# Performance work log

Measured on AMD Instinct MI355X. Metric: run time of the kernel, lower is better.

Reference implementation:

```python
import jax, jax.numpy as jnp
import numpy as np


def setup_inputs() -> dict:
    key = jax.random.key(0)
    k1, k2, k3, k4, k5 = jax.random.split(key, 5)
    D, K, W, C = 2048, 4096, 4096, 1000
    deep_feats = jax.random.normal(k1, (1, D), dtype=jnp.float32)
    cls_score = jax.random.normal(k2, (K, C), dtype=jnp.float32)
    target = jax.random.randint(k3, (1,), 0, C, dtype=jnp.int64)
    n = jax.random.normal(k4, (K, D), dtype=jnp.float32)
    w = jax.random.uniform(k5, (W, K), dtype=jnp.float32)
    return {"deep_feats": deep_feats, "cls_score": cls_score, "target": target, "n": n, "w": w}


def reference(deep_feats, cls_score, target, n, w):
    # d[idx] = ||deep_feats[0] - n[idx]||_2, shape [K]
    diff = deep_feats[0][None, :] - n            # [K, D]
    d = jnp.sqrt(jnp.sum(diff * diff, axis=-1))  # [K]
    # rho[idy] = softmax_idx(-w[idy] * d), shape [W, K]
    rho = jax.nn.softmax(-w * d[None, :], axis=-1)
    # f_loss = sum_{idy,idx} w[idy,idx] * d[idx]
    f_loss = jnp.sum(w * d[None, :])
    # per-neighbor cross entropy: ce[idx] = -log_softmax(cls_score[idx])[target]
    logp = jax.nn.log_softmax(cls_score, axis=-1)  # [K, C]
    ce = -logp[:, target[0]]                        # [K]
    # g_loss = sum_{idy,idx} rho[idy,idx] * ce[idx]
    g_loss = jnp.sum(rho @ ce)
    return g_loss + f_loss
```

## Files before the change

### kernel.cpp

```cpp
#include <hip/hip_runtime.h>
#include <math.h>

constexpr int KN = 4096;
constexpr int DN = 2048;
constexpr int CN = 1000;
constexpr int WN = 4096;

__device__ __forceinline__ float waveSum(float v) {
#pragma unroll
    for (int o = 32; o > 0; o >>= 1) v += __shfl_xor(v, o, 64);
    return v;
}
__device__ __forceinline__ float waveMax(float v) {
#pragma unroll
    for (int o = 32; o > 0; o >>= 1) v = fmaxf(v, __shfl_xor(v, o, 64));
    return v;
}

constexpr int S1_DIST_BLOCKS = KN / 4;
constexpr int S1_CE_BLOCKS   = KN / 4;

__global__ __launch_bounds__(256) void stage1_kernel(
    const float* __restrict__ deep, const float* __restrict__ nmat,
    const float* __restrict__ cls, const int* __restrict__ target,
    float* __restrict__ d_arr, float* __restrict__ ce_arr)
{
    const int b    = blockIdx.x;
    const int tid  = threadIdx.x;
    const int wv   = tid >> 6;
    const int lane = tid & 63;

    if (b < S1_DIST_BLOCKS) {
        const int row = b * 4 + wv;
        const float4* nrow = (const float4*)(nmat + (size_t)row * DN);
        const float4* df   = (const float4*)deep;
        float acc = 0.f;
#pragma unroll
        for (int c = 0; c < 8; ++c) {
            const int i = lane + 64 * c;
            const float4 a = df[i];
            const float4 x = nrow[i];
            const float e0 = a.x - x.x, e1 = a.y - x.y, e2 = a.z - x.z, e3 = a.w - x.w;
            acc += e0 * e0 + e1 * e1 + e2 * e2 + e3 * e3;
        }
        acc = waveSum(acc);
        if (lane == 0) d_arr[row] = sqrtf(acc);
    } else {
        const int row = (b - S1_DIST_BLOCKS) * 4 + wv;
        const float4* x4 = (const float4*)(cls + (size_t)row * CN);
        float4 v[4];
#pragma unroll
        for (int j = 0; j < 4; ++j) {
            const int i = lane + 64 * j;
            v[j] = (i < CN / 4) ? x4[i]
                                : make_float4(-INFINITY, -INFINITY, -INFINITY, -INFINITY);
        }
        float mx = -INFINITY;
#pragma unroll
        for (int j = 0; j < 4; ++j)
            mx = fmaxf(mx, fmaxf(fmaxf(v[j].x, v[j].y), fmaxf(v[j].z, v[j].w)));
        const float m = waveMax(mx);
        float s = 0.f;
#pragma unroll
        for (int j = 0; j < 4; ++j)
            s += __expf(v[j].x - m) + __expf(v[j].y - m)
               + __expf(v[j].z - m) + __expf(v[j].w - m);
        s = waveSum(s);
        if (lane == 0)
            ce_arr[row] = m + __logf(s) - cls[(size_t)row * CN + target[0]];
    }
}

constexpr int S2_BLOCK_THREADS = 512;
constexpr int S2_ROWS_PER_BLK  = 8;
constexpr int S2_BLOCKS        = WN / S2_ROWS_PER_BLK;

__global__ __launch_bounds__(S2_BLOCK_THREADS) void stage2_kernel(
    const float* __restrict__ wmat, const float* __restrict__ d_arr,
    const float* __restrict__ ce_arr, float* __restrict__ part)
{
    __shared__ float4 sd[KN / 4];
    __shared__ float4 sc[KN / 4];
    __shared__ float  wpart[8];

    const int tid  = threadIdx.x;
    const int wv   = tid >> 6;
    const int lane = tid & 63;

    {
        const float4* d4 = (const float4*)d_arr;
        const float4* c4 = (const float4*)ce_arr;
#pragma unroll
        for (int j = 0; j < 2; ++j) {
            const int i = tid + S2_BLOCK_THREADS * j;
            sd[i] = d4[i];
            sc[i] = c4[i];
        }
    }
    __syncthreads();

    const int row = blockIdx.x * S2_ROWS_PER_BLK + wv;
    const float4* wrow = (const float4*)(wmat + (size_t)row * KN);

    float es = 0.f, ec = 0.f, fs = 0.f;
#pragma unroll
    for (int c = 0; c < 16; ++c) {
        const int i = lane + 64 * c;
        const float4 a  = wrow[i];
        const float4 dv = sd[i];
        const float4 cv = sc[i];
        float t, e;
        t = a.x * dv.x; fs += t; e = __expf(-t); es += e; ec += e * cv.x;
        t = a.y * dv.y; fs += t; e = __expf(-t); es += e; ec += e * cv.y;
        t = a.z * dv.z; fs += t; e = __expf(-t); es += e; ec += e * cv.z;
        t = a.w * dv.w; fs += t; e = __expf(-t); es += e; ec += e * cv.w;
    }
    es = waveSum(es);  ec = waveSum(ec);  fs = waveSum(fs);

    if (lane == 0) wpart[wv] = ec / es + fs;
    __syncthreads();
    if (tid == 0) {
        float acc = 0.f;
#pragma unroll
        for (int j = 0; j < 8; ++j) acc += wpart[j];
        part[blockIdx.x] = acc;
    }
}

__global__ __launch_bounds__(S2_BLOCKS) void stage3_kernel(
    const float* __restrict__ part, float* __restrict__ out)
{
    __shared__ float red[8];
    const int tid  = threadIdx.x;
    const int wv   = tid >> 6;
    const int lane = tid & 63;
    float v = part[tid];
    v = waveSum(v);
    if (lane == 0) red[wv] = v;
    __syncthreads();
    if (tid == 0) {
        float acc = 0.f;
#pragma unroll
        for (int j = 0; j < 8; ++j) acc += red[j];
        out[0] = acc;
    }
}

extern "C" void kernel_launch(void* const* d_in, const int* in_sizes, int n_in,
                              void* d_out, int out_size, void* d_ws, size_t ws_size,
                              hipStream_t stream) {
    const float* deep   = (const float*)d_in[0];
    const float* cls    = (const float*)d_in[1];
    const int*   target = (const int*)d_in[2];
    const float* nmat   = (const float*)d_in[3];
    const float* wmat   = (const float*)d_in[4];

    float* ws     = (float*)d_ws;
    float* d_arr  = ws;
    float* ce_arr = ws + KN;
    float* part   = ws + 2 * KN;

    stage1_kernel<<<S1_DIST_BLOCKS + S1_CE_BLOCKS, 256, 0, stream>>>(
        deep, nmat, cls, target, d_arr, ce_arr);
    stage2_kernel<<<S2_BLOCKS, S2_BLOCK_THREADS, 0, stream>>>(
        wmat, d_arr, ce_arr, part);
    stage3_kernel<<<1, S2_BLOCKS, 0, stream>>>(part, (float*)d_out);
}
```

Baseline: 27.94 us.

## Drop LDS staging in stage2 and software-pipeline w-row loads with split accumulators

```diff
diff --git a/kernel.cpp b/kernel.cpp
--- a/kernel.cpp
+++ b/kernel.cpp
@@ -71,70 +71,72 @@
     }
 }
 
-constexpr int S2_BLOCK_THREADS = 512;
-constexpr int S2_ROWS_PER_BLK  = 8;
+constexpr int S2_BLOCK_THREADS = 256;
+constexpr int S2_ROWS_PER_BLK  = 4;
 constexpr int S2_BLOCKS        = WN / S2_ROWS_PER_BLK;
+constexpr int S2_NPART         = S2_BLOCKS;
 
-__global__ __launch_bounds__(S2_BLOCK_THREADS) void stage2_kernel(
+__global__ __launch_bounds__(S2_BLOCK_THREADS, 4) void stage2_kernel(
     const float* __restrict__ wmat, const float* __restrict__ d_arr,
     const float* __restrict__ ce_arr, float* __restrict__ part)
 {
-    __shared__ float4 sd[KN / 4];
-    __shared__ float4 sc[KN / 4];
-    __shared__ float  wpart[8];
-
+    __shared__ float wpart[4];
     const int tid  = threadIdx.x;
     const int wv   = tid >> 6;
     const int lane = tid & 63;
 
-    {
-        const float4* d4 = (const float4*)d_arr;
-        const float4* c4 = (const float4*)ce_arr;
-#pragma unroll
-        for (int j = 0; j < 2; ++j) {
-            const int i = tid + S2_BLOCK_THREADS * j;
-            sd[i] = d4[i];
-            sc[i] = c4[i];
-        }
-    }
-    __syncthreads();
-
     const int row = blockIdx.x * S2_ROWS_PER_BLK + wv;
     const float4* wrow = (const float4*)(wmat + (size_t)row * KN);
+    const float4* d4   = (const float4*)d_arr;
+    const float4* c4   = (const float4*)ce_arr;
 
-    float es = 0.f, ec = 0.f, fs = 0.f;
+    float4 wa[4], wb[4];
 #pragma unroll
-    for (int c = 0; c < 16; ++c) {
-        const int i = lane + 64 * c;
-        const float4 a  = wrow[i];
-        const float4 dv = sd[i];
-        const float4 cv = sc[i];
-        float t, e;
-        t = a.x * dv.x; fs += t; e = __expf(-t); es += e; ec += e * cv.x;
-        t = a.y * dv.y; fs += t; e = __expf(-t); es += e; ec += e * cv.y;
-        t = a.z * dv.z; fs += t; e = __expf(-t); es += e; ec += e * cv.z;
-        t = a.w * dv.w; fs += t; e = __expf(-t); es += e; ec += e * cv.w;
+    for (int j = 0; j < 4; ++j) wa[j] = wrow[lane + 64 * j];
+
+    float es0 = 0.f, ec0 = 0.f, fs0 = 0.f;
+    float es1 = 0.f, ec1 = 0.f, fs1 = 0.f;
+
+#pragma unroll
+    for (int c = 0; c < 16; c += 4) {
+        if (c + 4 < 16) {
+#pragma unroll
+            for (int j = 0; j < 4; ++j) wb[j] = wrow[lane + 64 * (c + 4 + j)];
+        }
+#pragma unroll
+        for (int j = 0; j < 4; ++j) {
+            const int i = lane + 64 * (c + j);
+            const float4 dv = d4[i];
+            const float4 cv = c4[i];
+            const float4 a  = wa[j];
+            float t, e;
+            t = a.x * dv.x; fs0 += t; e = __expf(-t); es0 += e; ec0 += e * cv.x;
+            t = a.y * dv.y; fs1 += t; e = __expf(-t); es1 += e; ec1 += e * cv.y;
+            t = a.z * dv.z; fs0 += t; e = __expf(-t); es0 += e; ec0 += e * cv.z;
+            t = a.w * dv.w; fs1 += t; e = __expf(-t); es1 += e; ec1 += e * cv.w;
+        }
+#pragma unroll
+        for (int j = 0; j < 4; ++j) wa[j] = wb[j];
     }
-    es = waveSum(es);  ec = waveSum(ec);  fs = waveSum(fs);
+
+    float es = waveSum(es0 + es1);
+    float ec = waveSum(ec0 + ec1);
+    float fs = waveSum(fs0 + fs1);
 
     if (lane == 0) wpart[wv] = ec / es + fs;
     __syncthreads();
-    if (tid == 0) {
-        float acc = 0.f;
-#pragma unroll
-        for (int j = 0; j < 8; ++j) acc += wpart[j];
-        part[blockIdx.x] = acc;
-    }
+    if (tid == 0)
+        part[blockIdx.x] = wpart[0] + wpart[1] + wpart[2] + wpart[3];
 }
 
-__global__ __launch_bounds__(S2_BLOCKS) void stage3_kernel(
+__global__ __launch_bounds__(512) void stage3_kernel(
     const float* __restrict__ part, float* __restrict__ out)
 {
     __shared__ float red[8];
     const int tid  = threadIdx.x;
     const int wv   = tid >> 6;
     const int lane = tid & 63;
-    float v = part[tid];
+    float v = part[tid] + part[tid + 512];
     v = waveSum(v);
     if (lane == 0) red[wv] = v;
     __syncthreads();
@@ -164,5 +166,5 @@
         deep, nmat, cls, target, d_arr, ce_arr);
     stage2_kernel<<<S2_BLOCKS, S2_BLOCK_THREADS, 0, stream>>>(
         wmat, d_arr, ce_arr, part);
-    stage3_kernel<<<1, S2_BLOCKS, 0, stream>>>(part, (float*)d_out);
+    stage3_kernel<<<1, 512, 0, stream>>>(part, (float*)d_out);
 }
```

Result: faster. 27.33 us (-2.2%).
